# Kernel tuning notes

Measured on AMD Instinct MI355X. Metric: run time of the kernel, lower is better.

## Reference

```python
import jax, jax.numpy as jnp
import numpy as np


def _overlap_add_fft_conv(signal, kernel):
    """Vectorized overlap-add FFT convolution.

    signal: (B, K, T) float; kernel: (B, K, R) float.
    Returns (B, K, T), identical math to the torch per-block loop (the
    ortho-normed rfft/irfft pair on the signal cancels, kernel rfft uses
    default backward norm, exactly as in the original code).
    """
    B, K, T = signal.shape
    R = kernel.shape[-1]
    fft_len = 2 << (R - 1).bit_length()          # e.g. R=4000 -> 8192
    step = fft_len - R + 1                        # hop between blocks
    pad_len = (-T) % step                         # pad T up to multiple of step
    L = T + pad_len
    n_blocks = L // step

    # split padded signal into non-overlapping blocks, zero-pad each to fft_len
    sig = jnp.pad(signal, ((0, 0), (0, 0), (0, pad_len)))
    blocks = sig.reshape(B, K, n_blocks, step)
    blocks = jnp.pad(blocks, ((0, 0), (0, 0), (0, 0), (0, fft_len - step)))

    kernel_fft = jnp.fft.rfft(
        jnp.pad(kernel, ((0, 0), (0, 0), (0, fft_len - R))))      # (B,K,F)
    block_fft = jnp.fft.rfft(blocks, norm='ortho')                # (B,K,n_blocks,F)
    conv = jnp.fft.irfft(block_fft * kernel_fft[:, :, None, :],
                         norm='ortho')                            # (B,K,n_blocks,fft_len)

    # overlap-add: block i contributes at offset i*step, length fft_len
    idx = jnp.arange(n_blocks)[:, None] * step + jnp.arange(fft_len)[None, :]
    out = jnp.zeros((B, K, L + R - 1), dtype=conv.dtype)
    out = out.at[:, :, idx].add(conv)
    return out[:, :, :T]


def setup_inputs() -> dict:
    key = jax.random.key(0)
    k1, k2 = jax.random.split(key)
    onsets = jax.random.normal(k1, (8, 8, 262144), dtype=jnp.float32)
    sources = jax.random.normal(k2, (8, 8, 4000), dtype=jnp.float32)
    return {"onsets": onsets, "sources": sources, "delay_compensation": 0}


def reference(onsets, sources, delay_compensation):
    # delay_compensation is unused in the original module as well
    return _overlap_add_fft_conv(onsets, sources)
```

## Files before the change

### kernel.cpp

```cpp
#include <hip/hip_runtime.h>

#define T_LEN 262144
#define R_LEN 4000
#define NCH 64
#define NCHUNK 253
#define WBLK 4616
#define SIG_M 145
#define LDS_BYTES 74240
#define NSTEP 272

typedef __attribute__((ext_vector_type(8))) short bf16x8;
typedef __attribute__((ext_vector_type(16))) float f32x16;

static __device__ __forceinline__ unsigned short f2bf(float f) {
  unsigned u = __builtin_bit_cast(unsigned, f);
  unsigned r = 0x7FFFu + ((u >> 16) & 1u);
  return (unsigned short)((u + r) >> 16);
}

__global__ __launch_bounds__(256) void build_btf(const float* __restrict__ src,
                                                 unsigned short* __restrict__ btf) {
  int t0 = blockIdx.x * 256 + threadIdx.x;
  if (t0 >= NCH * NCHUNK * 64) return;
  int lane = t0 & 63;
  int t = (t0 >> 6) % NCHUNK;
  int ch = t0 / (64 * NCHUNK);
  int j = lane & 31;
  int h = lane >> 5;
  int kbase = 4000 + j - 16 * t - 8 * h;
  const float* k = src + (size_t)ch * R_LEN;
  unsigned short vals[8];
#pragma unroll
  for (int e = 0; e < 8; ++e) {
    int r = kbase - e;
    float f = (r >= 0 && r < R_LEN) ? k[r] : 0.0f;
    vals[e] = f2bf(f);
  }
  unsigned int* dst = (unsigned int*)(btf + (size_t)t0 * 8);
  dst[0] = (unsigned int)vals[0] | ((unsigned int)vals[1] << 16);
  dst[1] = (unsigned int)vals[2] | ((unsigned int)vals[3] << 16);
  dst[2] = (unsigned int)vals[4] | ((unsigned int)vals[5] << 16);
  dst[3] = (unsigned int)vals[6] | ((unsigned int)vals[7] << 16);
}

__global__ __launch_bounds__(256, 2) void conv_main(const float* __restrict__ x,
                                                    const unsigned short* __restrict__ btf,
                                                    float* __restrict__ out) {
  __shared__ alignas(16) unsigned char xs[LDS_BYTES];
  const int bid = blockIdx.x;
  const int ch = bid & 63;
  const int T0 = (bid >> 6) << 15;
  const float* xch = x + (size_t)ch * T_LEN;
  const char* btc = (const char*)btf + (size_t)ch * NCHUNK * 1024;

  const int tid = threadIdx.x;
  const int lane = tid & 63;
  const int w = tid >> 6;

  for (int n = tid; n < WBLK; n += 256) {
    int gi = T0 - 4000 + 8 * n;
    float v0, v1, v2, v3, v4, v5, v6, v7;
    if (gi >= 0 && gi + 8 <= T_LEN) {
      float4 a = *(const float4*)(xch + gi);
      float4 b = *(const float4*)(xch + gi + 4);
      v0 = a.x; v1 = a.y; v2 = a.z; v3 = a.w;
      v4 = b.x; v5 = b.y; v6 = b.z; v7 = b.w;
    } else {
      v0 = (gi + 0 >= 0 && gi + 0 < T_LEN) ? xch[gi + 0] : 0.f;
      v1 = (gi + 1 >= 0 && gi + 1 < T_LEN) ? xch[gi + 1] : 0.f;
      v2 = (gi + 2 >= 0 && gi + 2 < T_LEN) ? xch[gi + 2] : 0.f;
      v3 = (gi + 3 >= 0 && gi + 3 < T_LEN) ? xch[gi + 3] : 0.f;
      v4 = (gi + 4 >= 0 && gi + 4 < T_LEN) ? xch[gi + 4] : 0.f;
      v5 = (gi + 5 >= 0 && gi + 5 < T_LEN) ? xch[gi + 5] : 0.f;
      v6 = (gi + 6 >= 0 && gi + 6 < T_LEN) ? xch[gi + 6] : 0.f;
      v7 = (gi + 7 >= 0 && gi + 7 < T_LEN) ? xch[gi + 7] : 0.f;
    }
    uint4 pk;
    pk.x = (unsigned int)f2bf(v0) | ((unsigned int)f2bf(v1) << 16);
    pk.y = (unsigned int)f2bf(v2) | ((unsigned int)f2bf(v3) << 16);
    pk.z = (unsigned int)f2bf(v4) | ((unsigned int)f2bf(v5) << 16);
    pk.w = (unsigned int)f2bf(v6) | ((unsigned int)f2bf(v7) << 16);
    int sig = (n >> 5) + SIG_M * (n & 31);
    *(uint4*)(xs + 16 * sig) = pk;
  }
  __syncthreads();

  const int l31 = lane & 31;
  const int h = lane >> 5;
  const unsigned abase = 16u * (32 * w + l31 + SIG_M * h);

  auto aread = [&](int q) -> bf16x8 {
    unsigned off = 16u * ((unsigned)(q >> 4) + 290u * (unsigned)(q & 15));
    return *(const bf16x8*)(xs + abase + off);
  };
  auto bloadc = [&](int t) -> bf16x8 {
    int tc = t > 252 ? 252 : t;
    return *(const bf16x8*)(btc + (size_t)tc * 1024 + lane * 16);
  };

  f32x16 acc[8] = {};
  bf16x8 zero8 = {};
  bf16x8 E0 = bloadc(0), E1 = zero8, E2 = zero8, E3 = zero8,
         E4 = zero8, E5 = zero8, E6 = zero8, E7 = zero8;
  bf16x8 O0 = bloadc(1), O1 = zero8, O2 = zero8, O3 = zero8,
         O4 = zero8, O5 = zero8, O6 = zero8, O7 = zero8;
  bf16x8 a_cur = aread(0);

#define DO_STEP(R0, R1, R2, R3, R4, R5, R6, R7, QQ)                                      \
  {                                                                                      \
    bf16x8 nb = bloadc((QQ) + 2);                                                        \
    bf16x8 an = aread((QQ) + 1);                                                         \
    __builtin_amdgcn_s_setprio(1);                                                       \
    acc[0] = __builtin_amdgcn_mfma_f32_32x32x16_bf16(a_cur, R0, acc[0], 0, 0, 0);        \
    acc[1] = __builtin_amdgcn_mfma_f32_32x32x16_bf16(a_cur, R1, acc[1], 0, 0, 0);        \
    acc[2] = __builtin_amdgcn_mfma_f32_32x32x16_bf16(a_cur, R2, acc[2], 0, 0, 0);        \
    acc[3] = __builtin_amdgcn_mfma_f32_32x32x16_bf16(a_cur, R3, acc[3], 0, 0, 0);        \
    acc[4] = __builtin_amdgcn_mfma_f32_32x32x16_bf16(a_cur, R4, acc[4], 0, 0, 0);        \
    acc[5] = __builtin_amdgcn_mfma_f32_32x32x16_bf16(a_cur, R5, acc[5], 0, 0, 0);        \
    acc[6] = __builtin_amdgcn_mfma_f32_32x32x16_bf16(a_cur, R6, acc[6], 0, 0, 0);        \
    acc[7] = __builtin_amdgcn_mfma_f32_32x32x16_bf16(a_cur, R7, acc[7], 0, 0, 0);        \
    __builtin_amdgcn_s_setprio(0);                                                       \
    R7 = R6; R6 = R5; R5 = R4; R4 = R3; R3 = R2; R2 = R1; R1 = R0; R0 = nb;              \
    a_cur = an;                                                                          \
  }

#pragma unroll 8
  for (int q = 0; q < NSTEP; q += 2) {
    DO_STEP(E0, E1, E2, E3, E4, E5, E6, E7, q);
    DO_STEP(O0, O1, O2, O3, O4, O5, O6, O7, q + 1);
  }
#undef DO_STEP

  float* och = out + (size_t)ch * T_LEN + T0 + 8192 * w;
#pragma unroll
  for (int c = 0; c < 8; ++c) {
#pragma unroll
    for (int r = 0; r < 16; ++r) {
      int irow = (r & 3) + 8 * (r >> 2) + 4 * h;
      och[256 * irow + 32 * c + l31] = acc[c][r];
    }
  }
}

extern "C" void kernel_launch(void* const* d_in, const int* in_sizes, int n_in,
                              void* d_out, int out_size, void* d_ws, size_t ws_size,
                              hipStream_t stream) {
  const float* onsets  = (const float*)d_in[0];
  const float* sources = (const float*)d_in[1];
  unsigned short* btf  = (unsigned short*)d_ws;
  float* out = (float*)d_out;

  int nthr = NCH * NCHUNK * 64;
  build_btf<<<(nthr + 255) / 256, 256, 0, stream>>>(sources, btf);
  conv_main<<<512, 256, 0, stream>>>(onsets, btf, out);
}
```

Before: 118.0 us.

## Split convolution into single-wave blocks with per-wave signal tiles

Each block is reduced from four waves covering 32K outputs to a single wave covering 8K outputs, giving 2048 blocks with small per-block LDS tiles instead of 512 large ones. The kernel band registers are preloaded from negative chunk indices instead of zeros, which trims the step count, and loads are now prefetched two steps ahead. The setprio hints are removed. This aims at better occupancy and load balance across CUs and deeper latency hiding, at the cost of more redundant halo loads of the signal and less LDS reuse across waves.

```diff
diff --git a/kernel.cpp b/kernel.cpp
--- a/kernel.cpp
+++ b/kernel.cpp
@@ -4,10 +4,9 @@
 #define R_LEN 4000
 #define NCH 64
 #define NCHUNK 253
-#define WBLK 4616
-#define SIG_M 145
-#define LDS_BYTES 74240
-#define NSTEP 272
+#define SIG_M 48
+#define NSLOT 1536
+#define NSTEP 266
 
 typedef __attribute__((ext_vector_type(8))) short bf16x8;
 typedef __attribute__((ext_vector_type(16))) float f32x16;
@@ -43,28 +42,29 @@
   dst[3] = (unsigned int)vals[6] | ((unsigned int)vals[7] << 16);
 }
 
-__global__ __launch_bounds__(256, 2) void conv_main(const float* __restrict__ x,
-                                                    const unsigned short* __restrict__ btf,
-                                                    float* __restrict__ out) {
-  __shared__ alignas(16) unsigned char xs[LDS_BYTES];
+__global__ __launch_bounds__(64, 2) void conv_main(const float* __restrict__ x,
+                                                   const unsigned short* __restrict__ btf,
+                                                   float* __restrict__ out) {
+  __shared__ alignas(16) unsigned char xs[NSLOT * 16];
   const int bid = blockIdx.x;
   const int ch = bid & 63;
-  const int T0 = (bid >> 6) << 15;
+  const int T0 = (bid >> 6) << 13;
   const float* xch = x + (size_t)ch * T_LEN;
   const char* btc = (const char*)btf + (size_t)ch * NCHUNK * 1024;
 
-  const int tid = threadIdx.x;
-  const int lane = tid & 63;
-  const int w = tid >> 6;
+  const int lane = threadIdx.x;
 
-  for (int n = tid; n < WBLK; n += 256) {
+  for (int sig = lane; sig < NSLOT; sig += 64) {
+    int b = sig / 48;
+    int a = sig - 48 * b;
+    int n = 32 * a + b;
     int gi = T0 - 4000 + 8 * n;
     float v0, v1, v2, v3, v4, v5, v6, v7;
     if (gi >= 0 && gi + 8 <= T_LEN) {
-      float4 a = *(const float4*)(xch + gi);
-      float4 b = *(const float4*)(xch + gi + 4);
-      v0 = a.x; v1 = a.y; v2 = a.z; v3 = a.w;
-      v4 = b.x; v5 = b.y; v6 = b.z; v7 = b.w;
+      float4 va = *(const float4*)(xch + gi);
+      float4 vb = *(const float4*)(xch + gi + 4);
+      v0 = va.x; v1 = va.y; v2 = va.z; v3 = va.w;
+      v4 = vb.x; v5 = vb.y; v6 = vb.z; v7 = vb.w;
     } else {
       v0 = (gi + 0 >= 0 && gi + 0 < T_LEN) ? xch[gi + 0] : 0.f;
       v1 = (gi + 1 >= 0 && gi + 1 < T_LEN) ? xch[gi + 1] : 0.f;
@@ -80,37 +80,36 @@
     pk.y = (unsigned int)f2bf(v2) | ((unsigned int)f2bf(v3) << 16);
     pk.z = (unsigned int)f2bf(v4) | ((unsigned int)f2bf(v5) << 16);
     pk.w = (unsigned int)f2bf(v6) | ((unsigned int)f2bf(v7) << 16);
-    int sig = (n >> 5) + SIG_M * (n & 31);
     *(uint4*)(xs + 16 * sig) = pk;
   }
   __syncthreads();
 
   const int l31 = lane & 31;
   const int h = lane >> 5;
-  const unsigned abase = 16u * (32 * w + l31 + SIG_M * h);
+  const unsigned abase = 16u * (unsigned)l31;
 
   auto aread = [&](int q) -> bf16x8 {
-    unsigned off = 16u * ((unsigned)(q >> 4) + 290u * (unsigned)(q & 15));
+    unsigned s = 2u * (unsigned)q + (unsigned)h;
+    unsigned off = 16u * ((s >> 5) + (unsigned)SIG_M * (s & 31));
     return *(const bf16x8*)(xs + abase + off);
   };
-  auto bloadc = [&](int t) -> bf16x8 {
-    int tc = t > 252 ? 252 : t;
+  auto bloadz = [&](int t) -> bf16x8 {
+    int tc = ((unsigned)t > 252u) ? 252 : t;
     return *(const bf16x8*)(btc + (size_t)tc * 1024 + lane * 16);
   };
 
   f32x16 acc[8] = {};
-  bf16x8 zero8 = {};
-  bf16x8 E0 = bloadc(0), E1 = zero8, E2 = zero8, E3 = zero8,
-         E4 = zero8, E5 = zero8, E6 = zero8, E7 = zero8;
-  bf16x8 O0 = bloadc(1), O1 = zero8, O2 = zero8, O3 = zero8,
-         O4 = zero8, O5 = zero8, O6 = zero8, O7 = zero8;
-  bf16x8 a_cur = aread(0);
+  bf16x8 E0 = bloadz(0), E1 = bloadz(-2),  E2 = bloadz(-4),  E3 = bloadz(-6),
+         E4 = bloadz(-8), E5 = bloadz(-10), E6 = bloadz(-12), E7 = bloadz(-14);
+  bf16x8 O0 = bloadz(1), O1 = bloadz(-1),  O2 = bloadz(-3),  O3 = bloadz(-5),
+         O4 = bloadz(-7), O5 = bloadz(-9), O6 = bloadz(-11), O7 = bloadz(-13);
+  bf16x8 pE = bloadz(2), pO = bloadz(3);
+  bf16x8 a_cur = aread(0), a_nxt = aread(1);
 
-#define DO_STEP(R0, R1, R2, R3, R4, R5, R6, R7, QQ)                                      \
+#define DO_STEP(R0, R1, R2, R3, R4, R5, R6, R7, PP, QQ)                                  \
   {                                                                                      \
-    bf16x8 nb = bloadc((QQ) + 2);                                                        \
-    bf16x8 an = aread((QQ) + 1);                                                         \
-    __builtin_amdgcn_s_setprio(1);                                                       \
+    bf16x8 nb = bloadz((QQ) + 4);                   \
+    bf16x8 an = aread((QQ) + 2);                                       \
     acc[0] = __builtin_amdgcn_mfma_f32_32x32x16_bf16(a_cur, R0, acc[0], 0, 0, 0);        \
     acc[1] = __builtin_amdgcn_mfma_f32_32x32x16_bf16(a_cur, R1, acc[1], 0, 0, 0);        \
     acc[2] = __builtin_amdgcn_mfma_f32_32x32x16_bf16(a_cur, R2, acc[2], 0, 0, 0);        \
@@ -119,19 +118,19 @@
     acc[5] = __builtin_amdgcn_mfma_f32_32x32x16_bf16(a_cur, R5, acc[5], 0, 0, 0);        \
     acc[6] = __builtin_amdgcn_mfma_f32_32x32x16_bf16(a_cur, R6, acc[6], 0, 0, 0);        \
     acc[7] = __builtin_amdgcn_mfma_f32_32x32x16_bf16(a_cur, R7, acc[7], 0, 0, 0);        \
-    __builtin_amdgcn_s_setprio(0);                                                       \
-    R7 = R6; R6 = R5; R5 = R4; R4 = R3; R3 = R2; R2 = R1; R1 = R0; R0 = nb;              \
-    a_cur = an;                                                                          \
+    R7 = R6; R6 = R5; R5 = R4; R4 = R3; R3 = R2; R2 = R1; R1 = R0;                       \
+    R0 = PP; PP = nb;                                                                    \
+    a_cur = a_nxt; a_nxt = an;                                                           \
   }
 
-#pragma unroll 8
+#pragma unroll 4
   for (int q = 0; q < NSTEP; q += 2) {
-    DO_STEP(E0, E1, E2, E3, E4, E5, E6, E7, q);
-    DO_STEP(O0, O1, O2, O3, O4, O5, O6, O7, q + 1);
+    DO_STEP(E0, E1, E2, E3, E4, E5, E6, E7, pE, q);
+    DO_STEP(O0, O1, O2, O3, O4, O5, O6, O7, pO, q + 1);
   }
 #undef DO_STEP
 
-  float* och = out + (size_t)ch * T_LEN + T0 + 8192 * w;
+  float* och = out + (size_t)ch * T_LEN + T0;
 #pragma unroll
   for (int c = 0; c < 8; ++c) {
 #pragma unroll
@@ -152,5 +151,5 @@
 
   int nthr = NCH * NCHUNK * 64;
   build_btf<<<(nthr + 255) / 256, 256, 0, stream>>>(sources, btf);
-  conv_main<<<512, 256, 0, stream>>>(onsets, btf, out);
+  conv_main<<<NCH * 32, 64, 0, stream>>>(onsets, btf, out);
 }
```

Result: slower. 151.5 us (+28.4%).
